# Kernel tuning notes

Measured on AMD Instinct MI355X. Metric: run time of the kernel, lower is better.

The kernel has to match this reference:

```python
import jax, jax.numpy as jnp
import numpy as np

NUM_ROUTES = 8 * 17 * 17  # 2312
NUM_CAPS = 10
OUT_CH = 16
IN_CH = 8


def squash(x, axis):
    sn = jnp.sum(x * x, axis=axis, keepdims=True)
    return sn * x / ((1.0 + sn) * jnp.sqrt(sn))


def setup_inputs() -> dict:
    key = jax.random.key(0)
    ks = jax.random.split(key, 11)
    B = 128
    data = jax.random.normal(ks[0], (B, 3, 49, 49), dtype=jnp.float32)
    conv_w = jax.random.normal(ks[1], (32, 3, 9, 9), dtype=jnp.float32) * 0.06
    conv_b = jax.random.normal(ks[2], (32,), dtype=jnp.float32) * 0.01
    # 8 primary-capsule convs, each 32->8, stacked: [8, 8, 32, 9, 9]
    prim_w = jax.random.normal(ks[3], (8, 8, 32, 9, 9), dtype=jnp.float32) * 0.02
    prim_b = jax.random.normal(ks[4], (8, 8), dtype=jnp.float32) * 0.01
    # DigitCaps W: torch used plain randn, shape [num_routes, num_caps, out, in]
    W_digit = jax.random.normal(ks[5], (NUM_ROUTES, NUM_CAPS, OUT_CH, IN_CH), dtype=jnp.float32)
    head_w1 = jax.random.normal(ks[6], (NUM_CAPS, 16, 100), dtype=jnp.float32) * 0.25
    head_b1 = jax.random.normal(ks[7], (NUM_CAPS, 100), dtype=jnp.float32) * 0.01
    head_w2 = jax.random.normal(ks[8], (NUM_CAPS, 100, 1), dtype=jnp.float32) * 0.1
    head_b2 = jax.random.normal(ks[9], (NUM_CAPS, 1), dtype=jnp.float32) * 0.01
    return {"data": data, "conv_w": conv_w, "conv_b": conv_b,
            "prim_w": prim_w, "prim_b": prim_b, "W_digit": W_digit,
            "head_w1": head_w1, "head_b1": head_b1,
            "head_w2": head_w2, "head_b2": head_b2}


def _forward(data, conv_w, conv_b, prim_w, prim_b, W_digit,
             head_w1, head_b1, head_w2, head_b2):
    dn = ("NCHW", "OIHW", "NCHW")
    # Conv stem: [B,3,49,49] -> [B,32,41,41], ReLU
    x = jax.lax.conv_general_dilated(data, conv_w, (1, 1), "VALID",
                                     dimension_numbers=dn)
    x = jax.nn.relu(x + conv_b[None, :, None, None])
    B = x.shape[0]
    # PrimaryCaps: 8 convs 32->8, k9 s2 -> [B,64,17,17] via merged weight
    pw = prim_w.reshape(64, 32, 9, 9)
    pb = prim_b.reshape(64)
    u = jax.lax.conv_general_dilated(x, pw, (2, 2), "VALID",
                                     dimension_numbers=dn)
    u = u + pb[None, :, None, None]
    u = u.reshape(B, 8, NUM_ROUTES)          # [B, 8 capsules, 2312]
    u = squash(u, axis=2)
    # DigitCaps: x_t [B, routes, in=8]; u_hat [B, routes, caps, out=16]
    x_t = u.transpose(0, 2, 1)
    u_hat = jnp.einsum("rcoi,bri->brco", W_digit, x_t)
    b_ij = jnp.zeros((NUM_ROUTES, NUM_CAPS), dtype=u_hat.dtype)
    v = None
    for it in range(3):
        c = jax.nn.softmax(b_ij, axis=1)                       # over capsules
        s = jnp.einsum("rc,brco->bco", c, u_hat)               # [B,caps,out]
        v = squash(s, axis=-1)                                 # [B,caps,16]
        if it < 2:
            a = jnp.einsum("brco,bco->brc", u_hat, v).mean(axis=0)
            b_ij = b_ij + a
    output = v[:, :, :, None]                                  # [B,10,16,1]
    # 10 tiny heads: head k applied to capsule k
    h = jnp.tanh(jnp.einsum("bci,cih->bch", v, head_w1) + head_b1[None])
    logits = jnp.einsum("bch,cho->bco", h, head_w2) + head_b2[None]
    cls = jax.nn.sigmoid(logits)                                # [B,10,1]
    return (output,) + tuple(cls[:, k] for k in range(NUM_CAPS))


def reference(data, conv_w, conv_b, prim_w, prim_b, W_digit,
              head_w1, head_b1, head_w2, head_b2):
    return _forward(data, conv_w, conv_b, prim_w, prim_b, W_digit,
                    head_w1, head_b1, head_w2, head_b2)
```

## Files before the change

kernel.cpp:

```cpp
#include <hip/hip_runtime.h>
#include <math.h>

#define BATCH 128
#define NR 2312
#define RC 34
#define NCH 68
#define NC 10
#define OC 16
#define IC 8
#define K1 352

typedef short short8 __attribute__((ext_vector_type(8)));
typedef float f32x4 __attribute__((ext_vector_type(4)));
typedef unsigned long long u64;

#define OFF_XH    0
#define OFF_U0    3442688
#define OFF_XTB   5810176
#define OFF_SC    6998016
#define OFF_BIJ   6999040
#define OFF_SP    7022160
#define OFF_V     8414800
#define OFF_WB    8435280
#define OFF_VT    8518224
#define OFF_W1    8538704

__device__ __forceinline__ unsigned short f2bf(float f) {
    unsigned int u = __float_as_uint(f);
    u = (u + 0x7FFFu + ((u >> 16) & 1u)) >> 16;
    return (unsigned short)u;
}
__device__ __forceinline__ float bf2f(unsigned short h) {
    return __uint_as_float(((unsigned int)h) << 16);
}

__global__ void k_prep(const float* __restrict__ cw, const float* __restrict__ pw,
                       unsigned short* __restrict__ W1, unsigned short* __restrict__ Wb,
                       float* __restrict__ bij, float* __restrict__ scale) {
    int idx = blockIdx.x * 256 + threadIdx.x;
    if (idx < 165888) {
        int ci = idx & 31, co = (idx >> 5) & 15, cog = (idx >> 9) & 3, tap = idx >> 11;
        Wb[idx] = f2bf(pw[((cog * 16 + co) * 32 + ci) * 81 + tap]);
        return;
    }
    idx -= 165888;
    if (idx < 23120) { bij[idx] = 0.f; return; }
    idx -= 23120;
    if (idx < 1024) { scale[idx] = 0.f; return; }
    idx -= 1024;
    if (idx < 32 * K1) {
        int co = idx / K1, k = idx - co * K1;
        int g = k / 12, kw = k - g * 12;
        float v = (kw < 9 && g < 27) ? cw[((co * 3 + g / 9) * 9 + (g % 9)) * 9 + kw] : 0.f;
        W1[idx] = f2bf(v);
    }
}

__global__ __launch_bounds__(512) void k_conv1m(const float* __restrict__ data,
                                                const unsigned short* __restrict__ W1,
                                                const float* __restrict__ cb,
                                                unsigned short* __restrict__ xh) {
    int b = blockIdx.x / 27, g64 = blockIdx.x % 27;
    int p0 = g64 * 64;
    int t = threadIdx.x, lane = t & 63, wv = t >> 6;
    int quad = lane >> 4, mloc = lane & 15;
    int msub = wv & 3, chh = wv >> 2;
    __shared__ __align__(16) unsigned short As[88 * 64 * 4];
    u64* ab = (u64*)As;
    for (int k = 81 * 64 + t; k < 88 * 64; k += 512) ab[k] = 0ull;
#pragma unroll 1
    for (int it = 0; it < 4; it++) {
        int g = wv + it * 8;
        if (g < 27) {
            int m = lane;
            int p = p0 + m; if (p > 1680) p = 1680;
            int h = p / 41, w = p - h * 41;
            int ci = g / 9, kh = g - ci * 9;
            const float* src = &data[((b * 3 + ci) * 49 + (h + kh)) * 49 + w];
            unsigned short pk[12];
#pragma unroll
            for (int kw = 0; kw < 9; kw++) pk[kw] = f2bf(src[kw]);
            pk[9] = 0; pk[10] = 0; pk[11] = 0;
            const u64* s = (const u64*)pk;
            ab[(3 * g + 0) * 64 + m] = s[0];
            ab[(3 * g + 1) * 64 + m] = s[1];
            ab[(3 * g + 2) * 64 + m] = s[2];
        }
    }
    __syncthreads();
    f32x4 acc = {0.f, 0.f, 0.f, 0.f};
    const unsigned short* wp = &W1[(size_t)(chh * 16 + mloc) * K1 + quad * 8];
    int mrow = msub * 16 + mloc;
#pragma unroll 1
    for (int kc = 0; kc < 11; kc++) {
        int c = kc * 8 + quad * 2;
        union { short8 v; u64 q[2]; } af;
        af.q[0] = ab[c * 64 + mrow];
        af.q[1] = ab[(c + 1) * 64 + mrow];
        short8 bfr = *(const short8*)(wp + kc * 32);
        acc = __builtin_amdgcn_mfma_f32_16x16x32_bf16(af.v, bfr, acc, 0, 0, 0);
    }
    __syncthreads();
    unsigned short* tile = As;
    float bias = cb[chh * 16 + mloc];
#pragma unroll
    for (int r = 0; r < 4; r++) {
        int m = msub * 16 + quad * 4 + r;
        float v0 = acc[r] + bias; v0 = v0 > 0.f ? v0 : 0.f;
        tile[m * 40 + chh * 16 + mloc] = f2bf(v0);
    }
    __syncthreads();
    if (t < 256) {
        int m = t >> 2, part = t & 3;
        int p = p0 + m;
        if (p < 1681)
            *(int4*)&xh[((size_t)(b * 1681 + p)) * 32 + part * 8] =
                *(const int4*)&tile[m * 40 + part * 8];
    }
}

__global__ __launch_bounds__(512) void k_conv2(const unsigned short* __restrict__ xh,
                                               const unsigned short* __restrict__ Wb,
                                               const float* __restrict__ pb,
                                               float* __restrict__ u0,
                                               float* __restrict__ scale) {
    int b = blockIdx.x / 5, g = blockIdx.x % 5;
    int t = threadIdx.x, lane = t & 63, wv = t >> 6;
    int quad = lane >> 4, mloc = lane & 15;
    int cg = wv & 3, half = wv >> 2;
    __shared__ __align__(16) char lds[50184];
    unsigned short* As = (unsigned short*)lds;
    const unsigned short* xb = xh + (size_t)b * 53792;
    int p_hi = g * 64 + 63; if (p_hi > 288) p_hi = 288;
    int r0 = 2 * ((g * 64) / 17);
    int nrows = 2 * (p_hi / 17) + 9 - r0;
    int nch = nrows * 164;
    for (int k = t; k < nch; k += 512) {
        int rl = k / 164, rem = k - rl * 164;
        int col = rem >> 2, ci8 = rem & 3;
        int e = (col & 1) ? 21 + (col >> 1) : (col >> 1);
        const u64* src = (const u64*)&xb[((r0 + rl) * 41 + col) * 32 + ci8 * 8];
        u64* dst = (u64*)&As[(rl * 41 + e) * 36 + ci8 * 8];
        dst[0] = src[0];
        dst[1] = src[1];
    }
    __syncthreads();
    int abase0, abase1;
    {
        int p = g * 64 + half * 32 + mloc;
        if (p > 288) p = 288;
        abase0 = ((2 * (p / 17) - r0) * 41 + (p % 17)) * 36 + quad * 8;
        p = g * 64 + half * 32 + 16 + mloc;
        if (p > 288) p = 288;
        abase1 = ((2 * (p / 17) - r0) * 41 + (p % 17)) * 36 + quad * 8;
    }
    const unsigned short* wbase = Wb + ((size_t)cg * 16 + mloc) * 32 + quad * 8;
    f32x4 acc0 = {0.f, 0.f, 0.f, 0.f}, acc1 = {0.f, 0.f, 0.f, 0.f};
#pragma unroll 1
    for (int kh = 0; kh < 9; kh++) {
        const unsigned short* wrow = wbase + (size_t)kh * 9 * 2048;
#pragma unroll
        for (int kw = 0; kw < 9; kw++) {
            short8 bf = *(const short8*)(wrow + (size_t)kw * 2048);
            int c0 = (kw & 1) ? 21 + (kw >> 1) : (kw >> 1);
            int off = (kh * 41 + c0) * 36;
            union { short8 v; u64 q[2]; } a0, a1;
            a0.q[0] = *(const u64*)&As[abase0 + off];
            a0.q[1] = *(const u64*)&As[abase0 + off + 4];
            a1.q[0] = *(const u64*)&As[abase1 + off];
            a1.q[1] = *(const u64*)&As[abase1 + off + 4];
            acc0 = __builtin_amdgcn_mfma_f32_16x16x32_bf16(a0.v, bf, acc0, 0, 0, 0);
            acc1 = __builtin_amdgcn_mfma_f32_16x16x32_bf16(a1.v, bf, acc1, 0, 0, 0);
        }
    }
    __syncthreads();
    float* tile = (float*)lds;
#pragma unroll
    for (int r = 0; r < 4; r++) {
        tile[(cg * 16 + mloc) * 65 + half * 32 + quad * 4 + r] = acc0[r];
        tile[(cg * 16 + mloc) * 65 + half * 32 + 16 + quad * 4 + r] = acc1[r];
    }
    __syncthreads();
    int co = t >> 3, p0 = (t & 7) * 8;
    float bias = pb[co];
    float ssum = 0.f;
#pragma unroll
    for (int j = 0; j < 8; j++) {
        int p = g * 64 + p0 + j;
        if (p < 289) {
            float val = tile[co * 65 + p0 + j] + bias;
            u0[((size_t)(b * 64 + co)) * 289 + p] = val;
            ssum += val * val;
        }
    }
#pragma unroll
    for (int d = 1; d < 64; d <<= 1) ssum += __shfl_xor(ssum, d);
    if (lane == 0) atomicAdd(&scale[b * 8 + wv], ssum);
}

__global__ __launch_bounds__(256) void k_xt(const float* __restrict__ u0,
                                            const float* __restrict__ scale,
                                            unsigned short* __restrict__ xTb) {
    int tid = blockIdx.x;
    int tile_i = tid / 10, hwt = tid % 10;
    int i = tile_i >> 3, j = tile_i & 7;
    int ch = i * 8 + j;
    int hw0 = hwt * 32;
    int rem = 289 - hw0; if (rem > 32) rem = 32;
    __shared__ float tile[32 * 130];
    __shared__ float sc_s[128];
    int t = threadIdx.x;
    if (t < 128) {
        float sn = scale[t * 8 + i];
        sc_s[t] = sn / ((1.f + sn) * sqrtf(sn));
    }
    for (int k = t; k < 32 * 128; k += 256) {
        int bb = k >> 5, x = k & 31;
        if (x < rem)
            tile[x * 130 + bb] = u0[(bb * 64 + ch) * 289 + hw0 + x];
    }
    __syncthreads();
    for (int k = t; k < 32 * 128; k += 256) {
        int hwl = k >> 7, bb = k & 127;
        if (hwl < rem)
            xTb[((size_t)((j * 289 + hw0 + hwl)) * 128 + bb) * 8 + i] =
                f2bf(tile[hwl * 130 + bb] * sc_s[bb]);
    }
}

__global__ __launch_bounds__(256) void k_s(const unsigned short* __restrict__ xTb,
                                           const float* __restrict__ W,
                                           const float* __restrict__ bij,
                                           float* __restrict__ spart) {
    int chunk = blockIdx.x / NC, c = blockIdx.x % NC;
    int r0 = chunk * RC;
    __shared__ __align__(16) unsigned short As[16 * 296];
    __shared__ float cs[RC];
    int t = threadIdx.x;
    { int o = t >> 4, kk = t & 15; As[o * 296 + 272 + kk] = 0; }
    if (t < RC) {
        int r = r0 + t;
        float x[NC], m = -1e30f;
#pragma unroll
        for (int k = 0; k < NC; k++) { x[k] = bij[r * NC + k]; m = fmaxf(m, x[k]); }
        float s = 0.f;
#pragma unroll
        for (int k = 0; k < NC; k++) { x[k] = expf(x[k] - m); s += x[k]; }
        cs[t] = x[c] / s;
    }
    __syncthreads();
    for (int k = t; k < RC * 16; k += 256) {
        int rr = k >> 4, o = k & 15;
        const float* wsrc = &W[(size_t)(r0 + rr) * 1280 + c * 128 + o * 8];
        float cr = cs[rr];
        unsigned short pk[8];
#pragma unroll
        for (int i = 0; i < 8; i++) pk[i] = f2bf(wsrc[i] * cr);
        *(int4*)&As[o * 296 + rr * 8] = *(const int4*)pk;
    }
    __syncthreads();
    int lane = t & 63, wv = t >> 6;
    int quad = lane >> 4, mloc = lane & 15;
    int n0 = wv * 32;
    f32x4 acc0 = {0.f, 0.f, 0.f, 0.f}, acc1 = {0.f, 0.f, 0.f, 0.f};
    const unsigned short* ap = &As[mloc * 296 + quad * 8];
#pragma unroll
    for (int kc = 0; kc < 9; kc++) {
        short8 af = *(const short8*)(ap + kc * 32);
        const unsigned short* bb = &xTb[(size_t)(r0 + kc * 4 + quad) * 1024];
        short8 b0 = *(const short8*)(bb + (n0 + mloc) * 8);
        short8 b1 = *(const short8*)(bb + (n0 + 16 + mloc) * 8);
        acc0 = __builtin_amdgcn_mfma_f32_16x16x32_bf16(af, b0, acc0, 0, 0, 0);
        acc1 = __builtin_amdgcn_mfma_f32_16x16x32_bf16(af, b1, acc1, 0, 0, 0);
    }
    float* sp = &spart[(size_t)(chunk * NC + c) * 2048];
    *(f32x4*)&sp[(n0 + mloc) * 16 + quad * 4] = acc0;
    *(f32x4*)&sp[(n0 + 16 + mloc) * 16 + quad * 4] = acc1;
}

__global__ __launch_bounds__(256) void k_v(const float* __restrict__ spart,
                    float* __restrict__ v, float* __restrict__ vT,
                    float* __restrict__ out,
                    const float* __restrict__ w1, const float* __restrict__ b1,
                    const float* __restrict__ w2, const float* __restrict__ b2,
                    int do_head) {
    int b = blockIdx.x / NC, c = blockIdx.x % NC;
    int t = threadIdx.x;
    int cl = t >> 4, o = t & 15;
    float s = 0.f;
#pragma unroll 1
    for (int ch = cl; ch < NCH; ch += 16)
        s += spart[((size_t)(ch * NC + c) * 128 + b) * 16 + o];
    s += __shfl_xor(s, 16);
    s += __shfl_xor(s, 32);
    __shared__ float red[4][16];
    __shared__ float hred[2];
    if ((t & 63) < 16) red[t >> 6][t & 15] = s;
    __syncthreads();
    if (t < 16) {
        float sum = red[0][t] + red[1][t] + red[2][t] + red[3][t];
        float sq = sum * sum;
#pragma unroll
        for (int d = 1; d < 16; d <<= 1) sq += __shfl_xor(sq, d);
        float vv = sum * sq / ((1.f + sq) * sqrtf(sq));
        int idx = (b * NC + c) * 16 + t;
        v[idx] = vv;
        out[idx] = vv;
        vT[(c * 16 + t) * 128 + b] = vv;
        red[0][t] = vv;
    }
    if (do_head) {
        __syncthreads();
        float partial = 0.f;
        if (t < 100) {
            float hs = b1[c * 100 + t];
#pragma unroll
            for (int i = 0; i < 16; i++) hs = fmaf(red[0][i], w1[(c * 16 + i) * 100 + t], hs);
            partial = tanhf(hs) * w2[c * 100 + t];
        }
#pragma unroll
        for (int d = 1; d < 64; d <<= 1) partial += __shfl_xor(partial, d);
        if ((t & 63) == 0 && t < 128) hred[t >> 6] = partial;
        __syncthreads();
        if (t == 0)
            out[20480 + c * 128 + b] = 1.f / (1.f + expf(-(hred[0] + hred[1] + b2[c])));
    }
}

__global__ __launch_bounds__(256) void k_a(const unsigned short* __restrict__ xTb,
                                           const float* __restrict__ W,
                                           const float* __restrict__ vT,
                                           float* __restrict__ bij) {
    int wv = threadIdx.x >> 6, lane = threadIdx.x & 63;
    int wid = __builtin_amdgcn_readfirstlane(blockIdx.x * 4 + wv);
    int r = wid / NC, c = wid - r * NC;
    const unsigned short* xr = &xTb[(size_t)r * 1024];
    union { short8 v; unsigned short u[8]; } s0, s1;
    s0.v = *(const short8*)(xr + lane * 8);
    s1.v = *(const short8*)(xr + (lane + 64) * 8);
    float x0[8], x1[8];
#pragma unroll
    for (int i = 0; i < 8; i++) { x0[i] = bf2f(s0.u[i]); x1[i] = bf2f(s1.u[i]); }
    const float* wr = &W[(size_t)r * 1280 + c * 128];
    const float* vc = &vT[c * 2048];
    float acc = 0.f;
#pragma unroll
    for (int o = 0; o < 16; o++) {
        float w[8];
#pragma unroll
        for (int i = 0; i < 8; i++) w[i] = wr[o * 8 + i];
        float u0 = 0.f, u1 = 0.f;
#pragma unroll
        for (int i = 0; i < 8; i++) { u0 = fmaf(w[i], x0[i], u0); u1 = fmaf(w[i], x1[i], u1); }
        acc = fmaf(vc[o * 128 + lane], u0, acc);
        acc = fmaf(vc[o * 128 + lane + 64], u1, acc);
    }
#pragma unroll
    for (int d = 1; d < 64; d <<= 1) acc += __shfl_xor(acc, d);
    if (lane == 0) bij[wid] += acc * 0.0078125f;
}

extern "C" void kernel_launch(void* const* d_in, const int* in_sizes, int n_in,
                              void* d_out, int out_size, void* d_ws, size_t ws_size,
                              hipStream_t stream) {
    const float* data   = (const float*)d_in[0];
    const float* conv_w = (const float*)d_in[1];
    const float* conv_b = (const float*)d_in[2];
    const float* prim_w = (const float*)d_in[3];
    const float* prim_b = (const float*)d_in[4];
    const float* Wd     = (const float*)d_in[5];
    const float* hw1    = (const float*)d_in[6];
    const float* hb1    = (const float*)d_in[7];
    const float* hw2    = (const float*)d_in[8];
    const float* hb2    = (const float*)d_in[9];
    float* ws = (float*)d_ws;
    unsigned short* xh  = (unsigned short*)(ws + OFF_XH);
    float* u0    = ws + OFF_U0;
    unsigned short* xTb = (unsigned short*)(ws + OFF_XTB);
    float* scale = ws + OFF_SC;
    float* bij   = ws + OFF_BIJ;
    float* spart = ws + OFF_SP;
    float* v     = ws + OFF_V;
    unsigned short* Wb  = (unsigned short*)(ws + OFF_WB);
    float* vT    = ws + OFF_VT;
    unsigned short* W1  = (unsigned short*)(ws + OFF_W1);
    float* out = (float*)d_out;

    k_prep<<<787, 256, 0, stream>>>(conv_w, prim_w, W1, Wb, bij, scale);
    k_conv1m<<<128 * 27, 512, 0, stream>>>(data, W1, conv_b, xh);
    k_conv2<<<128 * 5, 512, 0, stream>>>(xh, Wb, prim_b, u0, scale);
    k_xt<<<640, 256, 0, stream>>>(u0, scale, xTb);
    for (int it = 0; it < 3; it++) {
        k_s<<<NCH * NC, 256, 0, stream>>>(xTb, Wd, bij, spart);
        k_v<<<128 * NC, 256, 0, stream>>>(spart, v, vT, out, hw1, hb1, hw2, hb2,
                                          it == 2 ? 1 : 0);
        if (it < 2) k_a<<<5780, 256, 0, stream>>>(xTb, Wd, vT, bij);
    }
}
```

Before: 235.2 us.

## Fuse conv2 epilogue with bf16 transpose and split K across waves

The primary-capsule convolution now writes unscaled bf16 values straight into the transposed routing layout. This removes the fp32 u0 intermediate and the separate tiled transpose read. A light in-place kernel then applies the squash scale per batch and channel. The conv is retiled to 4 position groups of about 73 per batch, each wave doing 5 MFMA m-tiles, with the 9 kernel rows split between two wave halves and summed through LDS. The trade-offs are an extra bf16 rounding before scaling, which may change numerics slightly, and an extra LDS reduction pass.

```diff
diff --git a/kernel.cpp b/kernel.cpp
--- a/kernel.cpp
+++ b/kernel.cpp
@@ -6,8 +6,6 @@
 #define RC 34
 #define NCH 68
 #define NC 10
-#define OC 16
-#define IC 8
 #define K1 352
 
 typedef short short8 __attribute__((ext_vector_type(8)));
@@ -15,15 +13,14 @@
 typedef unsigned long long u64;
 
 #define OFF_XH    0
-#define OFF_U0    3442688
-#define OFF_XTB   5810176
-#define OFF_SC    6998016
-#define OFF_BIJ   6999040
-#define OFF_SP    7022160
-#define OFF_V     8414800
-#define OFF_WB    8435280
-#define OFF_VT    8518224
-#define OFF_W1    8538704
+#define OFF_XTB   3442688
+#define OFF_SC    4630528
+#define OFF_BIJ   4631552
+#define OFF_SP    4654672
+#define OFF_V     6047312
+#define OFF_WB    6067792
+#define OFF_VT    6150736
+#define OFF_W1    6171216
 
 __device__ __forceinline__ unsigned short f2bf(float f) {
     unsigned int u = __float_as_uint(f);
@@ -122,20 +119,21 @@
 __global__ __launch_bounds__(512) void k_conv2(const unsigned short* __restrict__ xh,
                                                const unsigned short* __restrict__ Wb,
                                                const float* __restrict__ pb,
-                                               float* __restrict__ u0,
+                                               unsigned short* __restrict__ xTb,
                                                float* __restrict__ scale) {
-    int b = blockIdx.x / 5, g = blockIdx.x % 5;
+    const int pstart[5] = {0, 73, 145, 217, 289};
+    int b = blockIdx.x >> 2, g = blockIdx.x & 3;
+    int p0 = pstart[g], np = pstart[g + 1] - p0;
+    int r0 = 2 * (p0 / 17);
     int t = threadIdx.x, lane = t & 63, wv = t >> 6;
     int quad = lane >> 4, mloc = lane & 15;
-    int cg = wv & 3, half = wv >> 2;
+    int cg = wv & 3, th = wv >> 2;
     __shared__ __align__(16) char lds[50184];
+    __shared__ float pbs[64];
     unsigned short* As = (unsigned short*)lds;
+    if (t < 64) pbs[t] = pb[t];
     const unsigned short* xb = xh + (size_t)b * 53792;
-    int p_hi = g * 64 + 63; if (p_hi > 288) p_hi = 288;
-    int r0 = 2 * ((g * 64) / 17);
-    int nrows = 2 * (p_hi / 17) + 9 - r0;
-    int nch = nrows * 164;
-    for (int k = t; k < nch; k += 512) {
+    for (int k = t; k < 17 * 164; k += 512) {
         int rl = k / 164, rem = k - rl * 164;
         int col = rem >> 2, ci8 = rem & 3;
         int e = (col & 1) ? 21 + (col >> 1) : (col >> 1);
@@ -145,87 +143,94 @@
         dst[1] = src[1];
     }
     __syncthreads();
-    int abase0, abase1;
-    {
-        int p = g * 64 + half * 32 + mloc;
+    int abase[5];
+#pragma unroll
+    for (int mt = 0; mt < 5; mt++) {
+        int p = p0 + mt * 16 + mloc;
         if (p > 288) p = 288;
-        abase0 = ((2 * (p / 17) - r0) * 41 + (p % 17)) * 36 + quad * 8;
-        p = g * 64 + half * 32 + 16 + mloc;
-        if (p > 288) p = 288;
-        abase1 = ((2 * (p / 17) - r0) * 41 + (p % 17)) * 36 + quad * 8;
+        abase[mt] = ((2 * (p / 17) - r0) * 41 + (p % 17)) * 36 + quad * 8;
     }
     const unsigned short* wbase = Wb + ((size_t)cg * 16 + mloc) * 32 + quad * 8;
-    f32x4 acc0 = {0.f, 0.f, 0.f, 0.f}, acc1 = {0.f, 0.f, 0.f, 0.f};
+    f32x4 acc[5];
+#pragma unroll
+    for (int mt = 0; mt < 5; mt++)
+#pragma unroll
+        for (int r = 0; r < 4; r++) acc[mt][r] = 0.f;
+    int kh0 = th ? 5 : 0, kh1 = th ? 9 : 5;
 #pragma unroll 1
-    for (int kh = 0; kh < 9; kh++) {
+    for (int kh = kh0; kh < kh1; kh++) {
         const unsigned short* wrow = wbase + (size_t)kh * 9 * 2048;
 #pragma unroll
         for (int kw = 0; kw < 9; kw++) {
             short8 bf = *(const short8*)(wrow + (size_t)kw * 2048);
             int c0 = (kw & 1) ? 21 + (kw >> 1) : (kw >> 1);
             int off = (kh * 41 + c0) * 36;
-            union { short8 v; u64 q[2]; } a0, a1;
-            a0.q[0] = *(const u64*)&As[abase0 + off];
-            a0.q[1] = *(const u64*)&As[abase0 + off + 4];
-            a1.q[0] = *(const u64*)&As[abase1 + off];
-            a1.q[1] = *(const u64*)&As[abase1 + off + 4];
-            acc0 = __builtin_amdgcn_mfma_f32_16x16x32_bf16(a0.v, bf, acc0, 0, 0, 0);
-            acc1 = __builtin_amdgcn_mfma_f32_16x16x32_bf16(a1.v, bf, acc1, 0, 0, 0);
+#pragma unroll
+            for (int mt = 0; mt < 5; mt++) {
+                union { short8 v; u64 q[2]; } a;
+                a.q[0] = *(const u64*)&As[abase[mt] + off];
+                a.q[1] = *(const u64*)&As[abase[mt] + off + 4];
+                acc[mt] = __builtin_amdgcn_mfma_f32_16x16x32_bf16(a.v, bf, acc[mt], 0, 0, 0);
+            }
         }
     }
     __syncthreads();
     float* tile = (float*)lds;
-#pragma unroll
-    for (int r = 0; r < 4; r++) {
-        tile[(cg * 16 + mloc) * 65 + half * 32 + quad * 4 + r] = acc0[r];
-        tile[(cg * 16 + mloc) * 65 + half * 32 + 16 + quad * 4 + r] = acc1[r];
-    }
-    __syncthreads();
-    int co = t >> 3, p0 = (t & 7) * 8;
-    float bias = pb[co];
-    float ssum = 0.f;
-#pragma unroll
-    for (int j = 0; j < 8; j++) {
-        int p = g * 64 + p0 + j;
-        if (p < 289) {
-            float val = tile[co * 65 + p0 + j] + bias;
-            u0[((size_t)(b * 64 + co)) * 289 + p] = val;
-            ssum += val * val;
+    if (th == 0) {
+#pragma unroll
+        for (int mt = 0; mt < 5; mt++)
+#pragma unroll
+            for (int r = 0; r < 4; r++)
+                tile[(cg * 16 + mloc) * 81 + mt * 16 + quad * 4 + r] = acc[mt][r];
+    }
+    __syncthreads();
+    if (th == 1) {
+#pragma unroll
+        for (int mt = 0; mt < 5; mt++)
+#pragma unroll
+            for (int r = 0; r < 4; r++)
+                tile[(cg * 16 + mloc) * 81 + mt * 16 + quad * 4 + r] += acc[mt][r];
+    }
+    __syncthreads();
+    float ssq[8] = {0.f, 0.f, 0.f, 0.f, 0.f, 0.f, 0.f, 0.f};
+#pragma unroll 1
+    for (int idx = t; idx < 8 * np; idx += 512) {
+        int pp = idx >> 3, j = idx & 7;
+        unsigned short pk[8];
+#pragma unroll
+        for (int i = 0; i < 8; i++) {
+            float val = tile[(i * 8 + j) * 81 + pp] + pbs[i * 8 + j];
+            pk[i] = f2bf(val);
+            ssq[i] += val * val;
         }
-    }
-#pragma unroll
-    for (int d = 1; d < 64; d <<= 1) ssum += __shfl_xor(ssum, d);
-    if (lane == 0) atomicAdd(&scale[b * 8 + wv], ssum);
-}
-
-__global__ __launch_bounds__(256) void k_xt(const float* __restrict__ u0,
-                                            const float* __restrict__ scale,
-                                            unsigned short* __restrict__ xTb) {
-    int tid = blockIdx.x;
-    int tile_i = tid / 10, hwt = tid % 10;
-    int i = tile_i >> 3, j = tile_i & 7;
-    int ch = i * 8 + j;
-    int hw0 = hwt * 32;
-    int rem = 289 - hw0; if (rem > 32) rem = 32;
-    __shared__ float tile[32 * 130];
-    __shared__ float sc_s[128];
+        *(int4*)&xTb[((size_t)(j * 289 + p0 + pp) * 128 + b) * 8] = *(const int4*)pk;
+    }
+#pragma unroll
+    for (int i = 0; i < 8; i++) {
+        float s = ssq[i];
+#pragma unroll
+        for (int d = 1; d < 64; d <<= 1) s += __shfl_xor(s, d);
+        if (lane == 0) atomicAdd(&scale[b * 8 + i], s);
+    }
+}
+
+__global__ __launch_bounds__(256) void k_xt(unsigned short* __restrict__ xTb,
+                                            const float* __restrict__ scale) {
+    __shared__ float fs[1024];
     int t = threadIdx.x;
-    if (t < 128) {
-        float sn = scale[t * 8 + i];
-        sc_s[t] = sn / ((1.f + sn) * sqrtf(sn));
-    }
-    for (int k = t; k < 32 * 128; k += 256) {
-        int bb = k >> 5, x = k & 31;
-        if (x < rem)
-            tile[x * 130 + bb] = u0[(bb * 64 + ch) * 289 + hw0 + x];
-    }
-    __syncthreads();
-    for (int k = t; k < 32 * 128; k += 256) {
-        int hwl = k >> 7, bb = k & 127;
-        if (hwl < rem)
-            xTb[((size_t)((j * 289 + hw0 + hwl)) * 128 + bb) * 8 + i] =
-                f2bf(tile[hwl * 130 + bb] * sc_s[bb]);
-    }
+    for (int k = t; k < 1024; k += 256) {
+        float sn = scale[k];
+        fs[k] = sn / ((1.f + sn) * sqrtf(sn));
+    }
+    __syncthreads();
+    int idx = blockIdx.x * 256 + t;
+    int b = idx & 127;
+    unsigned short* p = &xTb[(size_t)idx * 8];
+    union { int4 v; unsigned short u[8]; } d;
+    d.v = *(const int4*)p;
+#pragma unroll
+    for (int i = 0; i < 8; i++) d.u[i] = f2bf(bf2f(d.u[i]) * fs[b * 8 + i]);
+    *(int4*)p = d.v;
 }
 
 __global__ __launch_bounds__(256) void k_s(const unsigned short* __restrict__ xTb,
@@ -375,7 +380,6 @@
     const float* hb2    = (const float*)d_in[9];
     float* ws = (float*)d_ws;
     unsigned short* xh  = (unsigned short*)(ws + OFF_XH);
-    float* u0    = ws + OFF_U0;
     unsigned short* xTb = (unsigned short*)(ws + OFF_XTB);
     float* scale = ws + OFF_SC;
     float* bij   = ws + OFF_BIJ;
@@ -388,8 +392,8 @@
 
     k_prep<<<787, 256, 0, stream>>>(conv_w, prim_w, W1, Wb, bij, scale);
     k_conv1m<<<128 * 27, 512, 0, stream>>>(data, W1, conv_b, xh);
-    k_conv2<<<128 * 5, 512, 0, stream>>>(xh, Wb, prim_b, u0, scale);
-    k_xt<<<640, 256, 0, stream>>>(u0, scale, xTb);
+    k_conv2<<<128 * 4, 512, 0, stream>>>(xh, Wb, prim_b, xTb, scale);
+    k_xt<<<1156, 256, 0, stream>>>(xTb, scale);
     for (int it = 0; it < 3; it++) {
         k_s<<<NCH * NC, 256, 0, stream>>>(xTb, Wd, bij, spart);
         k_v<<<128 * NC, 256, 0, stream>>>(spart, v, vT, out, hw1, hb1, hw2, hb2,
```

Result: no change. 234.0 us (-0.5%).
